# Performance work log

Measured on AMD Instinct MI355X. Metric: run time of the kernel, lower is better.

## Reference

```python
import jax, jax.numpy as jnp
import numpy as np

D = 1024      # n_embd
H = 16        # n_head
DH = D // H   # head dim = 64
FF = 4 * D    # 4096
EPS = 1e-5
MASKED_BIAS = -10000.0


def gelu_new(x):
    # GPT-2 'gelu_new': 0.5*x*(1+tanh(sqrt(2/pi)*(x+0.044715*x^3)))
    c = np.sqrt(2.0 / np.pi).astype(np.float32)
    return 0.5 * x * (1.0 + jnp.tanh(c * (x + 0.044715 * x * x * x)))


def layer_norm(x, g, b):
    mu = jnp.mean(x, axis=-1, keepdims=True)
    var = jnp.mean(jnp.square(x - mu), axis=-1, keepdims=True)
    return (x - mu) * jax.lax.rsqrt(var + EPS) * g + b


def setup_inputs() -> dict:
    key = jax.random.key(0)
    ks = jax.random.split(key, 8)
    B, S = 4, 2048
    std = 0.02
    return {
        "hidden_states": jax.random.normal(ks[0], (B, S, D), jnp.float32),
        "ln1_g": jnp.ones((D,), jnp.float32),
        "ln1_b": jnp.zeros((D,), jnp.float32),
        "w_attn": std * jax.random.normal(ks[1], (D, 3 * D), jnp.float32),
        "b_attn": jnp.zeros((3 * D,), jnp.float32),
        "w_attn_proj": std * jax.random.normal(ks[2], (D, D), jnp.float32),
        "b_attn_proj": jnp.zeros((D,), jnp.float32),
        "ln2_g": jnp.ones((D,), jnp.float32),
        "ln2_b": jnp.zeros((D,), jnp.float32),
        "w_fc": std * jax.random.normal(ks[3], (D, FF), jnp.float32),
        "b_fc": jnp.zeros((FF,), jnp.float32),
        "w_mlp_proj": std * jax.random.normal(ks[4], (FF, D), jnp.float32),
        "b_mlp_proj": jnp.zeros((D,), jnp.float32),
    }


def reference(hidden_states, ln1_g, ln1_b, w_attn, b_attn, w_attn_proj, b_attn_proj,
              ln2_g, ln2_b, w_fc, b_fc, w_mlp_proj, b_mlp_proj):
    B, S, _ = hidden_states.shape

    # --- self-attention ---
    x = layer_norm(hidden_states, ln1_g, ln1_b)
    qkv = x @ w_attn + b_attn                       # [B,S,3D]
    q, k, v = jnp.split(qkv, 3, axis=-1)
    # split heads -> [B,H,S,DH]
    q = q.reshape(B, S, H, DH).transpose(0, 2, 1, 3)
    k = k.reshape(B, S, H, DH).transpose(0, 2, 1, 3)
    v = v.reshape(B, S, H, DH).transpose(0, 2, 1, 3)

    w = jnp.einsum('bhqd,bhkd->bhqk', q, k) / jnp.sqrt(jnp.float32(DH))
    causal = jnp.tril(jnp.ones((S, S), bool))       # [S,S]
    w = jnp.where(causal, w, jnp.float32(MASKED_BIAS))
    w = jax.nn.softmax(w, axis=-1)
    a = jnp.einsum('bhqk,bhkd->bhqd', w, v)         # [B,H,S,DH]
    a = a.transpose(0, 2, 1, 3).reshape(B, S, D)
    a = a @ w_attn_proj + b_attn_proj
    hidden_states = hidden_states + a

    # --- MLP ---
    m = layer_norm(hidden_states, ln2_g, ln2_b)
    m = gelu_new(m @ w_fc + b_fc) @ w_mlp_proj + b_mlp_proj
    return hidden_states + m
```

## Files before the change

kernel.cpp:

```cpp
#include <hip/hip_runtime.h>
#include <hip/hip_bf16.h>
#include <cstddef>

#define SEQ   2048
#define DMODEL 1024
#define NHEAD 16
#define HDIM  64
#define FFDIM 4096
#define QT    (SEQ / 64)

typedef __attribute__((ext_vector_type(8))) short bf16x8;
typedef __attribute__((ext_vector_type(4))) short bf16x4;
typedef __attribute__((ext_vector_type(4))) float f32x4;

#define QSCALE (0.125f * 1.44269504088896f)

__device__ __forceinline__ unsigned short f2b(float x) {
  __hip_bfloat16 h = __float2bfloat16(x);
  return __builtin_bit_cast(unsigned short, h);
}
__device__ __forceinline__ float b2f(short u) {
  unsigned x = ((unsigned)(unsigned short)u) << 16;
  return __builtin_bit_cast(float, x);
}
__device__ __forceinline__ void gl16(const short* g, short* l) {
  __builtin_amdgcn_global_load_lds(
      (const __attribute__((address_space(1))) void*)g,
      (__attribute__((address_space(3))) void*)l, 16, 0, 0);
}

__global__ __launch_bounds__(256)
void ln_kernel(const float* __restrict__ x, const float* __restrict__ g,
               const float* __restrict__ b, short* __restrict__ y) {
  const int row = blockIdx.x;
  const int t = threadIdx.x;
  const float* xr = x + (size_t)row * DMODEL;
  float4 v = *(const float4*)(xr + t * 4);
  float s = v.x + v.y + v.z + v.w;
  float q = v.x * v.x + v.y * v.y + v.z * v.z + v.w * v.w;
  #pragma unroll
  for (int off = 32; off; off >>= 1) {
    s += __shfl_xor(s, off);
    q += __shfl_xor(q, off);
  }
  __shared__ float ss[4], qq[4];
  if ((t & 63) == 0) { ss[t >> 6] = s; qq[t >> 6] = q; }
  __syncthreads();
  s = ss[0] + ss[1] + ss[2] + ss[3];
  q = qq[0] + qq[1] + qq[2] + qq[3];
  const float mean = s * (1.f / DMODEL);
  const float var = q * (1.f / DMODEL) - mean * mean;
  const float rstd = rsqrtf(var + 1e-5f);
  float4 gv = *(const float4*)(g + t * 4);
  float4 bv = *(const float4*)(b + t * 4);
  bf16x4 o;
  o[0] = (short)f2b((v.x - mean) * rstd * gv.x + bv.x);
  o[1] = (short)f2b((v.y - mean) * rstd * gv.y + bv.y);
  o[2] = (short)f2b((v.z - mean) * rstd * gv.z + bv.z);
  o[3] = (short)f2b((v.w - mean) * rstd * gv.w + bv.w);
  *(bf16x4*)(y + (size_t)row * DMODEL + t * 4) = o;
}

__device__ __forceinline__ float gelu_new_f(float x) {
  const float c = 0.7978845608028654f;
  float u = c * (x + 0.044715f * x * x * x);
  float e = __expf(2.f * u);
  float t = 1.f - 2.f / (e + 1.f);
  return 0.5f * x * (1.f + t);
}

__global__ __launch_bounds__(256)
void wconv4_kernel(const float* __restrict__ w0, short* __restrict__ t0,
                   const float* __restrict__ w1, short* __restrict__ t1,
                   const float* __restrict__ w2, short* __restrict__ t2,
                   const float* __restrict__ w3, short* __restrict__ t3,
                   const float* __restrict__ ba, float* __restrict__ bas) {
  int id = blockIdx.x;
  const int t = threadIdx.x;
  if (id == 3072) {
    #pragma unroll
    for (int i = t; i < 3072; i += 256)
      bas[i] = ba[i] * (i < 1024 ? QSCALE : 1.f);
    return;
  }
  const float* W; short* Wt; int K, N;
  float sc = 1.f;
  if (id < 768)       { W = w0; Wt = t0; K = 1024; N = 3072; }
  else if (id < 1024) { id -= 768;  W = w1; Wt = t1; K = 1024; N = 1024; }
  else if (id < 2048) { id -= 1024; W = w2; Wt = t2; K = 1024; N = 4096; }
  else                { id -= 2048; W = w3; Wt = t3; K = 4096; N = 1024; }
  const int nt = N >> 6;
  const int n0 = (id % nt) * 64, k0 = (id / nt) * 64;
  if (W == w0 && n0 < 1024) sc = QSCALE;
  __shared__ short tile[64][72];
  #pragma unroll
  for (int i = 0; i < 4; ++i) {
    const int row = i * 16 + (t >> 4);
    const int col4 = (t & 15) * 4;
    float4 v = *(const float4*)(W + (size_t)(k0 + row) * N + n0 + col4);
    tile[col4 + 0][row] = (short)f2b(v.x * sc);
    tile[col4 + 1][row] = (short)f2b(v.y * sc);
    tile[col4 + 2][row] = (short)f2b(v.z * sc);
    tile[col4 + 3][row] = (short)f2b(v.w * sc);
  }
  __syncthreads();
  #pragma unroll
  for (int i = 0; i < 2; ++i) {
    const int cc = t + i * 256;
    const int nr = cc >> 3, k8 = (cc & 7) * 8;
    bf16x8 vv;
    #pragma unroll
    for (int j = 0; j < 8; ++j) vv[j] = tile[nr][k8 + j];
    *(bf16x8*)(Wt + (size_t)(n0 + nr) * K + k0 + k8) = vv;
  }
}

template <bool OUTBF, bool GELU, bool RES, bool QKVS>
__global__ __launch_bounds__(256)
void gemm_bf16(const short* __restrict__ A, const short* __restrict__ Bt,
               const float* __restrict__ bias, const float* __restrict__ R,
               void* __restrict__ C, short* __restrict__ C2,
               short* __restrict__ C3, int M, int N, int K, int nbn) {
  __shared__ short As[2][128 * 64];
  __shared__ short Bs[2][128 * 64];
  const int t = threadIdx.x, lane = t & 63, w = t >> 6;
  const int g = lane >> 4, la = lane & 15;
  const int cpx = gridDim.x >> 3;
  const int swz = (blockIdx.x & 7) * cpx + (blockIdx.x >> 3);
  const int bn = swz % nbn, bm = swz / nbn;
  const int wm = w >> 1, wn = w & 1;

  const int srow = t >> 3;
  const int scolb = ((t & 7) * 16) ^ ((srow & 7) << 4);
  const short* Ag = A + (size_t)(bm * 128 + srow) * K + (scolb >> 1);
  const short* Bg = Bt + (size_t)(bn * 128 + srow) * K + (scolb >> 1);

  f32x4 acc[4][4];
  #pragma unroll
  for (int i = 0; i < 4; ++i)
    #pragma unroll
    for (int j = 0; j < 4; ++j) acc[i][j] = (f32x4){0.f, 0.f, 0.f, 0.f};

  const int KT = K >> 6;
  #pragma unroll
  for (int i = 0; i < 4; ++i) {
    gl16(Ag + (size_t)i * 32 * K, As[0] + i * 2048 + t * 8);
    gl16(Bg + (size_t)i * 32 * K, Bs[0] + i * 2048 + t * 8);
  }
  __syncthreads();

  int cur = 0;
  #pragma unroll 1
  for (int kt = 0; kt < KT; ++kt) {
    if (kt + 1 < KT) {
      #pragma unroll
      for (int i = 0; i < 4; ++i) {
        gl16(Ag + (size_t)i * 32 * K + (kt + 1) * 64,
             As[cur ^ 1] + i * 2048 + t * 8);
        gl16(Bg + (size_t)i * 32 * K + (kt + 1) * 64,
             Bs[cur ^ 1] + i * 2048 + t * 8);
      }
    }
    #pragma unroll
    for (int ks = 0; ks < 2; ++ks) {
      bf16x8 af[4], bfr[4];
      #pragma unroll
      for (int mi = 0; mi < 4; ++mi) {
        const int row = wm * 64 + mi * 16 + la;
        af[mi] = *(const bf16x8*)((const char*)As[cur] + row * 128 +
                                  ((ks * 64 + g * 16) ^ ((row & 7) << 4)));
      }
      #pragma unroll
      for (int ni = 0; ni < 4; ++ni) {
        const int row = wn * 64 + ni * 16 + la;
        bfr[ni] = *(const bf16x8*)((const char*)Bs[cur] + row * 128 +
                                   ((ks * 64 + g * 16) ^ ((row & 7) << 4)));
      }
      #pragma unroll
      for (int mi = 0; mi < 4; ++mi)
        #pragma unroll
        for (int ni = 0; ni < 4; ++ni)
          acc[mi][ni] = __builtin_amdgcn_mfma_f32_16x16x32_bf16(
              af[mi], bfr[ni], acc[mi][ni], 0, 0, 0);
    }
    __syncthreads();
    cur ^= 1;
  }

  const int crow0 = bm * 128 + wm * 64 + g * 4;
  const int ccol0 = bn * 128 + wn * 64 + la;
  float bl[4];
  #pragma unroll
  for (int ni = 0; ni < 4; ++ni) bl[ni] = bias[ccol0 + ni * 16];
  #pragma unroll
  for (int mi = 0; mi < 4; ++mi) {
    #pragma unroll
    for (int r = 0; r < 4; ++r) {
      const int row = crow0 + mi * 16 + r;
      if (QKVS) {
        const int bq = row >> 11, s = row & 2047;
        #pragma unroll
        for (int ni = 0; ni < 4; ++ni) {
          const int n = ccol0 + ni * 16;
          const int region = n >> 10;
          const int nn = n & 1023;
          short* dst = region == 0 ? (short*)C : (region == 1 ? C2 : C3);
          dst[((size_t)(bq * NHEAD + (nn >> 6)) * SEQ + s) * 64 + (nn & 63)] =
              (short)f2b(acc[mi][ni][r] + bl[ni]);
        }
      } else {
        #pragma unroll
        for (int ni = 0; ni < 4; ++ni) {
          float v = acc[mi][ni][r] + bl[ni];
          if (GELU) v = gelu_new_f(v);
          if (RES) v += R[(size_t)row * N + ccol0 + ni * 16];
          if (OUTBF)
            ((short*)C)[(size_t)row * N + ccol0 + ni * 16] = (short)f2b(v);
          else
            ((float*)C)[(size_t)row * N + ccol0 + ni * 16] = v;
        }
      }
    }
  }
}

__global__ __launch_bounds__(256)
void prepv_kernel(const short* __restrict__ Vb, short* __restrict__ Vtb) {
  const int st = blockIdx.x, h = blockIdx.y, b = blockIdx.z;
  const int t = threadIdx.x;
  const int s0 = st * 64;
  const size_t bh = (size_t)b * NHEAD + h;
  __shared__ short vt[64][72];
  #pragma unroll
  for (int i = 0; i < 2; ++i) {
    const int cc = t + i * 256;
    const int r = cc >> 3, d8 = (cc & 7) * 8;
    bf16x8 v8 = *(const bf16x8*)(Vb + (bh * SEQ + s0 + r) * 64 + d8);
    #pragma unroll
    for (int j = 0; j < 8; ++j) vt[d8 + j][r] = v8[j];
  }
  __syncthreads();
  #pragma unroll
  for (int i = 0; i < 2; ++i) {
    const int cc = t + i * 256;
    const int d = cc >> 3, s8 = (cc & 7) * 8;
    bf16x8 vv;
    #pragma unroll
    for (int j = 0; j < 8; ++j) vv[j] = vt[d][s8 + j];
    *(bf16x8*)(Vtb + (bh * 64 + d) * SEQ + s0 + s8) = vv;
  }
}

__global__ __launch_bounds__(256)
void mha_kernel(const short* __restrict__ Qb, const short* __restrict__ Kb,
                const short* __restrict__ Vtb, short* __restrict__ out) {
  const int p = blockIdx.x, h = blockIdx.y, b = blockIdx.z;
  const int t = threadIdx.x, lane = t & 63, w = t >> 6;
  const int g = lane >> 4, la = lane & 15;
  const size_t bh = (size_t)b * NHEAD + h;

  __shared__ short Ks[2][64 * 64];
  __shared__ short Vts[2][64 * 64];
  __shared__ short Ps[4][16 * 64];

  const int srow = t >> 3;
  const int scolb = ((t & 7) * 16) ^ ((srow & 7) << 4);

  const int qt0 = p, qt1 = QT - 1 - p;
  const int T0 = qt0 + 1, total = T0 + qt1 + 1;

  int qt = qt0;
  const short* qr = Qb + (bh * SEQ + (size_t)qt0 * 64 + w * 16 + la) * 64;
  bf16x8 qf0 = *(const bf16x8*)(qr + g * 8);
  bf16x8 qf1 = *(const bf16x8*)(qr + 32 + g * 8);

  float o[16];
  #pragma unroll
  for (int i = 0; i < 16; ++i) o[i] = 0.f;
  float m = -1e30f, l = 0.f;

  #pragma unroll
  for (int i = 0; i < 2; ++i) {
    const int r = srow + i * 32;
    gl16(Kb + (bh * SEQ + r) * 64 + (scolb >> 1), Ks[0] + i * 2048 + t * 8);
    gl16(Vtb + (bh * 64 + r) * SEQ + (scolb >> 1), Vts[0] + i * 2048 + t * 8);
  }
  __syncthreads();

  int cur = 0;
  #pragma unroll 1
  for (int it = 0; it < total; ++it) {
    if (it + 1 < total) {
      const int nkt = (it + 1 < T0) ? (it + 1) : (it + 1 - T0);
      const int nk0 = nkt * 64;
      #pragma unroll
      for (int i = 0; i < 2; ++i) {
        const int r = srow + i * 32;
        gl16(Kb + (bh * SEQ + nk0 + r) * 64 + (scolb >> 1),
             Ks[cur ^ 1] + i * 2048 + t * 8);
        gl16(Vtb + (bh * 64 + r) * SEQ + nk0 + (scolb >> 1),
             Vts[cur ^ 1] + i * 2048 + t * 8);
      }
    }

    float sv[16];
    __builtin_amdgcn_s_setprio(1);
    #pragma unroll
    for (int mt = 0; mt < 4; ++mt) {
      const int ar = mt * 16 + la;
      const int ab = ar * 128 + ((g * 16) ^ ((ar & 7) << 4));
      bf16x8 ka0 = *(const bf16x8*)((char*)Ks[cur] + ab);
      bf16x8 ka1 = *(const bf16x8*)((char*)Ks[cur] + (ab ^ 64));
      f32x4 sa = {0.f, 0.f, 0.f, 0.f};
      sa = __builtin_amdgcn_mfma_f32_16x16x32_bf16(ka0, qf0, sa, 0, 0, 0);
      sa = __builtin_amdgcn_mfma_f32_16x16x32_bf16(ka1, qf1, sa, 0, 0, 0);
      sv[mt * 4 + 0] = sa[0]; sv[mt * 4 + 1] = sa[1];
      sv[mt * 4 + 2] = sa[2]; sv[mt * 4 + 3] = sa[3];
    }
    __builtin_amdgcn_s_setprio(0);

    const bool diag = (it == T0 - 1) || (it == total - 1);
    if (diag) {
      const int qrel = w * 16 + la;
      #pragma unroll
      for (int idx = 0; idx < 16; ++idx) {
        const int krel = (idx >> 2) * 16 + g * 4 + (idx & 3);
        if (krel > qrel) sv[idx] = -14426.950408889634f;
      }
    }

    float t8[8], t4[4], t2[2];
    #pragma unroll
    for (int i = 0; i < 8; ++i) t8[i] = fmaxf(sv[2 * i], sv[2 * i + 1]);
    #pragma unroll
    for (int i = 0; i < 4; ++i) t4[i] = fmaxf(t8[2 * i], t8[2 * i + 1]);
    t2[0] = fmaxf(t4[0], t4[1]); t2[1] = fmaxf(t4[2], t4[3]);
    float tmax = fmaxf(t2[0], t2[1]);
    tmax = fmaxf(tmax, __shfl_xor(tmax, 16));
    tmax = fmaxf(tmax, __shfl_xor(tmax, 32));

    const bool skip = __all(tmax <= m + 11.5f) != 0;
    const float mn = skip ? m : fmaxf(m, tmax);

    float ss8[8], ss4[4];
    #pragma unroll
    for (int i = 0; i < 16; ++i) sv[i] = exp2f(sv[i] - mn);
    #pragma unroll
    for (int i = 0; i < 8; ++i) ss8[i] = sv[2 * i] + sv[2 * i + 1];
    #pragma unroll
    for (int i = 0; i < 4; ++i) ss4[i] = ss8[2 * i] + ss8[2 * i + 1];
    float ps = (ss4[0] + ss4[1]) + (ss4[2] + ss4[3]);
    ps += __shfl_xor(ps, 16);
    ps += __shfl_xor(ps, 32);

    if (skip) {
      l += ps;
    } else {
      const float sc = exp2f(m - mn);
      l = l * sc + ps;
      m = mn;
      #pragma unroll
      for (int r = 0; r < 4; ++r) {
        const float scr = __shfl(sc, (g << 2) + r);
        o[r] *= scr; o[4 + r] *= scr; o[8 + r] *= scr; o[12 + r] *= scr;
      }
    }

    #pragma unroll
    for (int mt = 0; mt < 4; ++mt) {
      #pragma unroll
      for (int r2 = 0; r2 < 2; ++r2) {
        const unsigned pk = (unsigned)f2b(sv[mt * 4 + r2 * 2]) |
                            ((unsigned)f2b(sv[mt * 4 + r2 * 2 + 1]) << 16);
        const int kk = mt * 16 + g * 4 + r2 * 2;
        const int pb = la * 128 + ((kk * 2) ^ ((la & 7) << 4));
        *(unsigned*)((char*)Ps[w] + pb) = pk;
      }
    }
    asm volatile("s_waitcnt lgkmcnt(0)" ::: "memory");
    __builtin_amdgcn_sched_barrier(0);

    const int pb0 = la * 128 + ((g * 16) ^ ((la & 7) << 4));
    const bf16x8 pa0 = *(const bf16x8*)((char*)Ps[w] + pb0);
    const bf16x8 pa1 = *(const bf16x8*)((char*)Ps[w] + (pb0 ^ 64));
    __builtin_amdgcn_s_setprio(1);
    #pragma unroll
    for (int nt = 0; nt < 4; ++nt) {
      const int dr = nt * 16 + la;
      const int vb = dr * 128 + ((g * 16) ^ ((dr & 7) << 4));
      bf16x8 vb0 = *(const bf16x8*)((char*)Vts[cur] + vb);
      bf16x8 vb1 = *(const bf16x8*)((char*)Vts[cur] + (vb ^ 64));
      f32x4 oa = {o[nt * 4 + 0], o[nt * 4 + 1], o[nt * 4 + 2], o[nt * 4 + 3]};
      oa = __builtin_amdgcn_mfma_f32_16x16x32_bf16(pa0, vb0, oa, 0, 0, 0);
      oa = __builtin_amdgcn_mfma_f32_16x16x32_bf16(pa1, vb1, oa, 0, 0, 0);
      o[nt * 4 + 0] = oa[0]; o[nt * 4 + 1] = oa[1];
      o[nt * 4 + 2] = oa[2]; o[nt * 4 + 3] = oa[3];
    }
    __builtin_amdgcn_s_setprio(0);

    if (diag) {
      const float linv = 1.f / l;
      #pragma unroll
      for (int r = 0; r < 4; ++r) {
        const float li = __shfl(linv, (g << 2) + r);
        const int qrow_g = qt * 64 + w * 16 + g * 4 + r;
        #pragma unroll
        for (int nt = 0; nt < 4; ++nt) {
          out[((size_t)b * SEQ + qrow_g) * DMODEL + h * 64 + nt * 16 + la] =
              (short)f2b(o[nt * 4 + r] * li);
        }
      }
      if (it == T0 - 1) {
        #pragma unroll
        for (int i = 0; i < 16; ++i) o[i] = 0.f;
        m = -1e30f; l = 0.f;
        qt = qt1;
        const short* qr1 = Qb + (bh * SEQ + (size_t)qt1 * 64 + w * 16 + la) * 64;
        qf0 = *(const bf16x8*)(qr1 + g * 8);
        qf1 = *(const bf16x8*)(qr1 + 32 + g * 8);
      }
    }

    __syncthreads();
    cur ^= 1;
  }
}

extern "C" void kernel_launch(void* const* d_in, const int* in_sizes, int n_in,
                              void* d_out, int out_size, void* d_ws, size_t ws_size,
                              hipStream_t stream) {
  const float* hidden      = (const float*)d_in[0];
  const float* ln1_g       = (const float*)d_in[1];
  const float* ln1_b       = (const float*)d_in[2];
  const float* w_attn      = (const float*)d_in[3];
  const float* b_attn      = (const float*)d_in[4];
  const float* w_attn_proj = (const float*)d_in[5];
  const float* b_attn_proj = (const float*)d_in[6];
  const float* ln2_g       = (const float*)d_in[7];
  const float* ln2_b       = (const float*)d_in[8];
  const float* w_fc        = (const float*)d_in[9];
  const float* b_fc        = (const float*)d_in[10];
  const float* w_mlp_proj  = (const float*)d_in[11];
  const float* b_mlp_proj  = (const float*)d_in[12];
  float* out = (float*)d_out;

  const int Bn = in_sizes[0] / (SEQ * DMODEL);
  const int M = Bn * SEQ;

  char* W = (char*)d_ws;
  const size_t szMD2 = (size_t)M * DMODEL * 2;
  short* xln_b  = (short*)W;
  short* Vb     = (short*)(W + szMD2);
  short* a1_b   = Vb;
  char*  p2     = W + szMD2 + (size_t)M * FFDIM * 2;
  short* Qb     = (short*)p2;
  short* Kb     = Qb + (size_t)M * DMODEL;
  short* Vtb    = Kb + (size_t)M * DMODEL;
  short* attn_b = Vtb + (size_t)M * DMODEL;
  float* h2     = (float*)(p2 + 4 * szMD2);
  short* wat    = (short*)(p2 + 4 * szMD2 + (size_t)M * DMODEL * 4);
  short* wpt    = wat + (size_t)3 * DMODEL * DMODEL;
  short* wft    = wpt + (size_t)DMODEL * DMODEL;
  short* wmt    = wft + (size_t)FFDIM * DMODEL;
  float* bas    = (float*)(wmt + (size_t)DMODEL * FFDIM);

  wconv4_kernel<<<3073, 256, 0, stream>>>(w_attn, wat, w_attn_proj, wpt,
                                          w_fc, wft, w_mlp_proj, wmt,
                                          b_attn, bas);
  ln_kernel<<<M, 256, 0, stream>>>(hidden, ln1_g, ln1_b, xln_b);
  gemm_bf16<true, false, false, true><<<24 * 64, 256, 0, stream>>>(
      xln_b, wat, bas, nullptr, Qb, Kb, Vb, M, 3 * DMODEL, DMODEL, 24);
  prepv_kernel<<<dim3(SEQ / 64, NHEAD, Bn), 256, 0, stream>>>(Vb, Vtb);
  mha_kernel<<<dim3(QT / 2, NHEAD, Bn), 256, 0, stream>>>(Qb, Kb, Vtb, attn_b);
  gemm_bf16<false, false, true, false><<<8 * 64, 256, 0, stream>>>(
      attn_b, wpt, b_attn_proj, hidden, h2, nullptr, nullptr, M, DMODEL, DMODEL, 8);
  ln_kernel<<<M, 256, 0, stream>>>(h2, ln2_g, ln2_b, xln_b);
  gemm_bf16<true, true, false, false><<<32 * 64, 256, 0, stream>>>(
      xln_b, wft, b_fc, nullptr, a1_b, nullptr, nullptr, M, FFDIM, DMODEL, 32);
  gemm_bf16<false, false, true, false><<<8 * 64, 256, 0, stream>>>(
      a1_b, wmt, b_mlp_proj, h2, out, nullptr, nullptr, M, DMODEL, FFDIM, 8);
}
```

Baseline: 507.2 us.

## Switch GEMM to triple-buffered 32-wide K stages with fine-grained waitcnt barriers

Rewrites the bf16 GEMM main loop from a double-buffered 64-wide K tile to a three-stage ring of 32-wide K tiles. Loads run two stages ahead, and explicit s_waitcnt vmcnt plus s_barrier replaces __syncthreads, so global loads overlap compute without draining. A new XOR swizzle matches the 64-byte rows, and s_setprio raises priority around the MFMA block. Each iteration now has half the MFMA work to hide barrier and load latency, which costs more barriers per K and risks exposing latency.

```diff
diff --git a/kernel.cpp b/kernel.cpp
--- a/kernel.cpp
+++ b/kernel.cpp
@@ -121,8 +121,8 @@
                const float* __restrict__ bias, const float* __restrict__ R,
                void* __restrict__ C, short* __restrict__ C2,
                short* __restrict__ C3, int M, int N, int K, int nbn) {
-  __shared__ short As[2][128 * 64];
-  __shared__ short Bs[2][128 * 64];
+  __shared__ short As[3][128 * 32];
+  __shared__ short Bs[3][128 * 32];
   const int t = threadIdx.x, lane = t & 63, w = t >> 6;
   const int g = lane >> 4, la = lane & 15;
   const int cpx = gridDim.x >> 3;
@@ -130,10 +130,12 @@
   const int bn = swz % nbn, bm = swz / nbn;
   const int wm = w >> 1, wn = w & 1;
 
-  const int srow = t >> 3;
-  const int scolb = ((t & 7) * 16) ^ ((srow & 7) << 4);
-  const short* Ag = A + (size_t)(bm * 128 + srow) * K + (scolb >> 1);
-  const short* Bg = Bt + (size_t)(bn * 128 + srow) * K + (scolb >> 1);
+  const int r0 = t >> 2;
+  const int sca = ((t & 3) ^ ((r0 >> 1) & 3)) * 8;
+  const short* Ag0 = A + (size_t)(bm * 128 + r0) * K + sca;
+  const short* Ag1 = A + (size_t)(bm * 128 + r0 + 64) * K + sca;
+  const short* Bg0 = Bt + (size_t)(bn * 128 + r0) * K + sca;
+  const short* Bg1 = Bt + (size_t)(bn * 128 + r0 + 64) * K + sca;
 
   f32x4 acc[4][4];
   #pragma unroll
@@ -141,51 +143,58 @@
     #pragma unroll
     for (int j = 0; j < 4; ++j) acc[i][j] = (f32x4){0.f, 0.f, 0.f, 0.f};
 
-  const int KT = K >> 6;
-  #pragma unroll
-  for (int i = 0; i < 4; ++i) {
-    gl16(Ag + (size_t)i * 32 * K, As[0] + i * 2048 + t * 8);
-    gl16(Bg + (size_t)i * 32 * K, Bs[0] + i * 2048 + t * 8);
-  }
-  __syncthreads();
-
-  int cur = 0;
+  const int KT = K >> 5;
+  #define STAGE_G(buf, kt)                                   \
+    do {                                                     \
+      gl16(Ag0 + (kt) * 32, As[buf] + t * 8);                \
+      gl16(Ag1 + (kt) * 32, As[buf] + 2048 + t * 8);         \
+      gl16(Bg0 + (kt) * 32, Bs[buf] + t * 8);                \
+      gl16(Bg1 + (kt) * 32, Bs[buf] + 2048 + t * 8);         \
+    } while (0)
+
+  STAGE_G(0, 0);
+  STAGE_G(1, 1);
+  asm volatile("s_waitcnt vmcnt(4)\n\ts_barrier" ::: "memory");
+  __builtin_amdgcn_sched_barrier(0);
+
+  int bcur = 0;
   #pragma unroll 1
   for (int kt = 0; kt < KT; ++kt) {
-    if (kt + 1 < KT) {
-      #pragma unroll
-      for (int i = 0; i < 4; ++i) {
-        gl16(Ag + (size_t)i * 32 * K + (kt + 1) * 64,
-             As[cur ^ 1] + i * 2048 + t * 8);
-        gl16(Bg + (size_t)i * 32 * K + (kt + 1) * 64,
-             Bs[cur ^ 1] + i * 2048 + t * 8);
-      }
-    }
-    #pragma unroll
-    for (int ks = 0; ks < 2; ++ks) {
-      bf16x8 af[4], bfr[4];
-      #pragma unroll
-      for (int mi = 0; mi < 4; ++mi) {
-        const int row = wm * 64 + mi * 16 + la;
-        af[mi] = *(const bf16x8*)((const char*)As[cur] + row * 128 +
-                                  ((ks * 64 + g * 16) ^ ((row & 7) << 4)));
-      }
-      #pragma unroll
-      for (int ni = 0; ni < 4; ++ni) {
-        const int row = wn * 64 + ni * 16 + la;
-        bfr[ni] = *(const bf16x8*)((const char*)Bs[cur] + row * 128 +
-                                   ((ks * 64 + g * 16) ^ ((row & 7) << 4)));
-      }
-      #pragma unroll
-      for (int mi = 0; mi < 4; ++mi)
-        #pragma unroll
-        for (int ni = 0; ni < 4; ++ni)
-          acc[mi][ni] = __builtin_amdgcn_mfma_f32_16x16x32_bf16(
-              af[mi], bfr[ni], acc[mi][ni], 0, 0, 0);
-    }
-    __syncthreads();
-    cur ^= 1;
-  }
+    if (kt + 2 < KT) {
+      const int btgt = bcur == 0 ? 2 : bcur - 1;
+      STAGE_G(btgt, kt + 2);
+    }
+    bf16x8 af[4], bfr[4];
+    #pragma unroll
+    for (int mi = 0; mi < 4; ++mi) {
+      const int row = wm * 64 + mi * 16 + la;
+      af[mi] = *(const bf16x8*)((const char*)As[bcur] + row * 64 +
+                                ((g ^ ((row >> 1) & 3)) << 4));
+    }
+    #pragma unroll
+    for (int ni = 0; ni < 4; ++ni) {
+      const int row = wn * 64 + ni * 16 + la;
+      bfr[ni] = *(const bf16x8*)((const char*)Bs[bcur] + row * 64 +
+                                 ((g ^ ((row >> 1) & 3)) << 4));
+    }
+    __builtin_amdgcn_s_setprio(1);
+    #pragma unroll
+    for (int mi = 0; mi < 4; ++mi)
+      #pragma unroll
+      for (int ni = 0; ni < 4; ++ni)
+        acc[mi][ni] = __builtin_amdgcn_mfma_f32_16x16x32_bf16(
+            af[mi], bfr[ni], acc[mi][ni], 0, 0, 0);
+    __builtin_amdgcn_s_setprio(0);
+
+    if (kt < KT - 2) {
+      asm volatile("s_waitcnt vmcnt(4)\n\ts_barrier" ::: "memory");
+    } else if (kt == KT - 2) {
+      asm volatile("s_waitcnt vmcnt(0)\n\ts_barrier" ::: "memory");
+    }
+    __builtin_amdgcn_sched_barrier(0);
+    bcur = bcur == 2 ? 0 : bcur + 1;
+  }
+  #undef STAGE_G
 
   const int crow0 = bm * 128 + wm * 64 + g * 4;
   const int ccol0 = bn * 128 + wn * 64 + la;
```

Measured after the change: 532.1 us. 1.05x slower.

## Prefetch two K-tiles ahead in GEMM with fine-grained vmcnt waits and MFMA priority

Applied to the files above, without the earlier changes.

Restructures the GEMM main loop so global-to-LDS loads for tile kt+2 are issued right after the compute on tile kt, with two stages kept in flight. Explicit s_waitcnt vmcnt(8) plus s_barrier replaces __syncthreads, so each wave waits only for the current tile's loads, not the prefetch. s_setprio raises wave priority around the MFMA block. The aim is better overlap of global load latency with compute. It depends on exact vmcnt accounting and on scheduling barriers that limit compiler reordering.

```diff
diff --git a/kernel.cpp b/kernel.cpp
--- a/kernel.cpp
+++ b/kernel.cpp
@@ -142,28 +142,31 @@
     for (int j = 0; j < 4; ++j) acc[i][j] = (f32x4){0.f, 0.f, 0.f, 0.f};
 
   const int KT = K >> 6;
-  #pragma unroll
-  for (int i = 0; i < 4; ++i) {
-    gl16(Ag + (size_t)i * 32 * K, As[0] + i * 2048 + t * 8);
-    gl16(Bg + (size_t)i * 32 * K, Bs[0] + i * 2048 + t * 8);
-  }
-  __syncthreads();
+  #define STAGE_G(buf, kt)                                                  \
+    do {                                                                    \
+      _Pragma("unroll")                                                     \
+      for (int i = 0; i < 4; ++i) {                                         \
+        gl16(Ag + (size_t)i * 32 * K + (kt) * 64, As[buf] + i * 2048 + t * 8); \
+        gl16(Bg + (size_t)i * 32 * K + (kt) * 64, Bs[buf] + i * 2048 + t * 8); \
+      }                                                                     \
+    } while (0)
+
+  STAGE_G(0, 0);
+  STAGE_G(1, 1);
 
   int cur = 0;
   #pragma unroll 1
   for (int kt = 0; kt < KT; ++kt) {
     if (kt + 1 < KT) {
-      #pragma unroll
-      for (int i = 0; i < 4; ++i) {
-        gl16(Ag + (size_t)i * 32 * K + (kt + 1) * 64,
-             As[cur ^ 1] + i * 2048 + t * 8);
-        gl16(Bg + (size_t)i * 32 * K + (kt + 1) * 64,
-             Bs[cur ^ 1] + i * 2048 + t * 8);
-      }
-    }
+      asm volatile("s_waitcnt vmcnt(8)\n\ts_barrier" ::: "memory");
+    } else {
+      asm volatile("s_waitcnt vmcnt(0)\n\ts_barrier" ::: "memory");
+    }
+    __builtin_amdgcn_sched_barrier(0);
+
+    bf16x8 af[4], bfr[4];
     #pragma unroll
     for (int ks = 0; ks < 2; ++ks) {
-      bf16x8 af[4], bfr[4];
       #pragma unroll
       for (int mi = 0; mi < 4; ++mi) {
         const int row = wm * 64 + mi * 16 + la;
@@ -176,16 +179,22 @@
         bfr[ni] = *(const bf16x8*)((const char*)Bs[cur] + row * 128 +
                                    ((ks * 64 + g * 16) ^ ((row & 7) << 4)));
       }
+      __builtin_amdgcn_s_setprio(1);
       #pragma unroll
       for (int mi = 0; mi < 4; ++mi)
         #pragma unroll
         for (int ni = 0; ni < 4; ++ni)
           acc[mi][ni] = __builtin_amdgcn_mfma_f32_16x16x32_bf16(
               af[mi], bfr[ni], acc[mi][ni], 0, 0, 0);
-    }
-    __syncthreads();
+      __builtin_amdgcn_s_setprio(0);
+    }
+
+    asm volatile("s_barrier" ::: "memory");
+    __builtin_amdgcn_sched_barrier(0);
+    if (kt + 2 < KT) STAGE_G(cur, kt + 2);
     cur ^= 1;
   }
+  #undef STAGE_G
 
   const int crow0 = bm * 128 + wm * 64 + g * 4;
   const int ccol0 = bn * 128 + wn * 64 + la;
```

Measured after the change: 510.9 us. No clear change (+0.7%).
